# Performance work log

Hardware: AMD Instinct MI355X
Metric: run time of the kernel (lower is better)

The kernel has to match this reference:

```python
import jax, jax.numpy as jnp
import numpy as np

N, E, IN, H, HEADS, L, OUT = 4096, 262144, 64, 128, 4, 2, 2
DH = H // HEADS  # 32, per-head dim for both GAT and global MHA
BN_EPS = 1e-5
NEG_SLOPE = 0.2  # GATConv leaky_relu default


def setup_inputs() -> dict:
    key = jax.random.key(0)
    ks = iter(jax.random.split(key, 32))
    rn = lambda shape, s: jax.random.normal(next(ks), shape, jnp.float32) * s
    return {
        "x": rn((N, IN), 1.0),
        "edge_index": jax.random.randint(next(ks), (2, E), 0, N),
        "w_in": rn((H, IN), IN ** -0.5),
        "b_in": rn((H,), 0.02),
        "w_gat": rn((L, H, H), H ** -0.5),
        "att_src": rn((L, HEADS, DH), 0.1),
        "att_dst": rn((L, HEADS, DH), 0.1),
        "b_gat": rn((L, H), 0.02),
        "w_qkv": rn((L, 3 * H, H), H ** -0.5),
        "b_qkv": rn((L, 3 * H), 0.02),
        "w_o": rn((L, H, H), H ** -0.5),
        "b_o": rn((L, H), 0.02),
        "bn_gamma": 1.0 + rn((L, 3, H), 0.05),
        "bn_beta": rn((L, 3, H), 0.05),
        "w1": rn((L, 2 * H, H), H ** -0.5),
        "b1": rn((L, 2 * H), 0.02),
        "w2": rn((L, H, 2 * H), (2 * H) ** -0.5),
        "b2": rn((L, H), 0.02),
        "w_out": rn((OUT, H), H ** -0.5),
        "b_out": rn((OUT,), 0.02),
    }


def _bn(h, g, b):
    # eval-mode BatchNorm1d with running_mean=0, running_var=1
    return h * (g / jnp.sqrt(1.0 + BN_EPS)) + b


def _gat(x, src, dst, w, a_src, a_dst, bias):
    # GATConv(hidden, hidden//heads, heads=HEADS, add_self_loops=False), concat=True
    xp = (x @ w.T).reshape(N, HEADS, DH)                  # [N, HEADS, DH]
    al_s = jnp.einsum('nhd,hd->nh', xp, a_src)            # [N, HEADS]
    al_d = jnp.einsum('nhd,hd->nh', xp, a_dst)
    logit = al_s[src] + al_d[dst]                         # [E, HEADS]
    logit = jnp.where(logit >= 0, logit, NEG_SLOPE * logit)
    m = jax.ops.segment_max(logit, dst, num_segments=N)   # scatter-softmax over dst
    m = jnp.where(jnp.isfinite(m), m, 0.0)
    e = jnp.exp(logit - m[dst])
    denom = jax.ops.segment_sum(e, dst, num_segments=N)
    alpha = e / (denom[dst] + 1e-16)
    out = jax.ops.segment_sum(alpha[:, :, None] * xp[src], dst, num_segments=N)
    return out.reshape(N, H) + bias


def _mha(x, wqkv, bqkv, wo, bo):
    # torch.nn.MultiheadAttention self-attention over all N nodes (one graph)
    qkv = x @ wqkv.T + bqkv
    q, k, v = jnp.split(qkv, 3, axis=-1)
    q = q.reshape(N, HEADS, DH)
    k = k.reshape(N, HEADS, DH)
    v = v.reshape(N, HEADS, DH)
    scores = jnp.einsum('nhd,mhd->hnm', q, k) / jnp.sqrt(jnp.float32(DH))
    attn = jax.nn.softmax(scores, axis=-1)
    out = jnp.einsum('hnm,mhd->nhd', attn, v).reshape(N, H)
    return out @ wo.T + bo


def reference(x, edge_index, w_in, b_in, w_gat, att_src, att_dst, b_gat,
              w_qkv, b_qkv, w_o, b_o, bn_gamma, bn_beta,
              w1, b1, w2, b2, w_out, b_out):
    src, dst = edge_index[0], edge_index[1]
    h = jax.nn.relu(x @ w_in.T + b_in)
    for l in range(L):
        # GPSConv: local GAT branch (dropout inactive in eval)
        h_loc = _gat(h, src, dst, w_gat[l], att_src[l], att_dst[l], b_gat[l]) + h
        h_loc = _bn(h_loc, bn_gamma[l, 0], bn_beta[l, 0])
        # GPSConv: global attention branch
        h_att = _mha(h, w_qkv[l], b_qkv[l], w_o[l], b_o[l]) + h
        h_att = _bn(h_att, bn_gamma[l, 1], bn_beta[l, 1])
        out = h_loc + h_att
        mlp = jax.nn.relu(out @ w1[l].T + b1[l]) @ w2[l].T + b2[l]
        out = _bn(out + mlp, bn_gamma[l, 2], bn_beta[l, 2])
        # GPSRiskModel residual + relu (dropout inactive in eval)
        h = jax.nn.relu(out + h)
    return h @ w_out.T + b_out
```

## Files before the change

### kernel.cpp

```cpp
#include <hip/hip_runtime.h>

#define NN 4096
#define EE 262144
#define INF_ 64
#define HH 128
#define HEADS 4
#define DH 32
#define LL 2
#define NH (NN * HH)
#define KSPLIT 16
#define L2E 1.4426950408889634f

typedef unsigned short u16;
typedef unsigned int u32;
using bf16x8 = __attribute__((ext_vector_type(8))) short;
using f32x4 = __attribute__((ext_vector_type(4))) float;

__device__ __forceinline__ float bf2f(u16 v) { return __uint_as_float(((u32)v) << 16); }
__device__ __forceinline__ u16 f2bf(float f) {
    u32 u = __float_as_uint(f);
    u32 r = (u + 0x7fffu + ((u >> 16) & 1u)) >> 16;
    return (u16)r;
}
__device__ __forceinline__ u32 encf(float f) {
    u32 b = __float_as_uint(f);
    return (b & 0x80000000u) ? ~b : (b | 0x80000000u);
}
__device__ __forceinline__ float decf(u32 u) {
    u32 b = (u & 0x80000000u) ? (u & 0x7fffffffu) : ~u;
    return __uint_as_float(b);
}

__global__ __launch_bounds__(256) void k_detect(const u16* __restrict__ x, int* __restrict__ flag,
                                                int* __restrict__ cnt, u32* __restrict__ gmax) {
    int t = threadIdx.x;
    for (int i = t; i < NN; i += 256) cnt[i] = 0;
    if (t < 16) gmax[t] = 0;
    __shared__ int cs[256];
    u16 v = x[2 * t];
    int e = (v >> 7) & 0xFF;
    cs[t] = (e >= 100 && e <= 140) ? 1 : 0;
    __syncthreads();
    for (int s = 128; s > 0; s >>= 1) {
        if (t < s) cs[t] += cs[t + s];
        __syncthreads();
    }
    if (t == 0) *flag = (cs[0] >= 128) ? 1 : 0;
}

#define MAXSEG 16
struct SegF { const void* src[MAXSEG]; int dst[MAXSEG]; int n[MAXSEG]; int cnt; };
struct SegB { const void* src[8]; u16* dst[8]; u16* dst2[8]; int n[8]; int cnt; };
__global__ __launch_bounds__(256) void k_prep(SegF SF, float* __restrict__ W, SegB SB,
                                              const int* __restrict__ flag,
                                              const int* __restrict__ dst, int* __restrict__ cnt) {
    int bid = blockIdx.x, t = threadIdx.x;
    if (bid < 96) {
        int seg = bid >> 3, bx = bid & 7;
        if (seg >= SF.cnt) return;
        int n = SF.n[seg];
        float* d = W + SF.dst[seg];
        const void* s = SF.src[seg];
        int f = *flag;
        for (int i = bx * 256 + t; i < n; i += 8 * 256)
            d[i] = f ? bf2f(((const u16*)s)[i]) : ((const float*)s)[i];
    } else if (bid < 992) {
        int b2 = bid - 96;
        int seg = b2 >> 7, bx = b2 & 127;
        if (seg >= SB.cnt) return;
        int f = *flag;
        u16* d = SB.dst[seg];
        u16* d2 = SB.dst2[seg];
        if (f && !d2) return;
        int n = SB.n[seg];
        const void* s = SB.src[seg];
        for (int i = bx * 256 + t; i < n; i += 128 * 256) {
            if (d2) {
                float v = f ? bf2f(((const u16*)s)[i]) : ((const float*)s)[i];
                u16 h = f2bf(v);
                d[i] = h;
                d2[i] = f2bf(v - bf2f(h));
            } else {
                d[i] = f2bf(((const float*)s)[i]);
            }
        }
    } else {
        int e = (bid - 992) * 256 + t;
        if (e < EE) atomicAdd(&cnt[dst[e]], 1);
    }
}

__global__ __launch_bounds__(128) void k_mgemm(const u16* __restrict__ Ahi, const u16* __restrict__ Alo,
                                               const u16* __restrict__ Wc, const u16* __restrict__ Wd,
                                               const int* __restrict__ flag,
                                               const float* __restrict__ bias,
                                               float* __restrict__ outf, u16* __restrict__ outb16,
                                               u16* __restrict__ outhi, u16* __restrict__ outlo,
                                               int K, int J, int relu, int jtiles,
                                               const int* __restrict__ scnt, int* __restrict__ srowstart,
                                               int* __restrict__ scursor) {
    __shared__ int part[128];
    if ((int)blockIdx.y >= jtiles) {
        if (blockIdx.x != 0 || scnt == nullptr) return;
        int t = threadIdx.x;
        int loc[32];
        int s = 0;
#pragma unroll
        for (int i = 0; i < 32; ++i) { loc[i] = s; s += scnt[t * 32 + i]; }
        part[t] = s;
        __syncthreads();
        for (int off = 1; off < 128; off <<= 1) {
            int v = part[t];
            int a = (t >= off) ? part[t - off] : 0;
            __syncthreads();
            part[t] = v + a;
            __syncthreads();
        }
        int base = (t == 0) ? 0 : part[t - 1];
#pragma unroll
        for (int i = 0; i < 32; ++i) {
            srowstart[t * 32 + i] = base + loc[i];
            scursor[t * 32 + i] = base + loc[i];
        }
        return;
    }
    const u16* Wb = (*flag) ? Wd : Wc;
    int wave = threadIdx.x >> 6, lane = threadIdx.x & 63;
    int grp = lane >> 4, lcol = lane & 15;
    int m0 = blockIdx.x * 32 + wave * 16;
    int j0 = blockIdx.y * 64;
    f32x4 acc[4];
#pragma unroll
    for (int s = 0; s < 4; ++s) acc[s] = (f32x4){0.f, 0.f, 0.f, 0.f};
    const u16* ah = Ahi + (size_t)(m0 + lcol) * K + grp * 8;
    const u16* al = Alo + (size_t)(m0 + lcol) * K + grp * 8;
    const u16* wb = Wb + (size_t)(j0 + lcol) * K + grp * 8;
    for (int k = 0; k < K; k += 32) {
        bf16x8 va = *(const bf16x8*)(ah + k);
        bf16x8 vl = *(const bf16x8*)(al + k);
#pragma unroll
        for (int s = 0; s < 4; ++s) {
            bf16x8 vw = *(const bf16x8*)(wb + (size_t)s * 16 * K + k);
            acc[s] = __builtin_amdgcn_mfma_f32_16x16x32_bf16(va, vw, acc[s], 0, 0, 0);
            acc[s] = __builtin_amdgcn_mfma_f32_16x16x32_bf16(vl, vw, acc[s], 0, 0, 0);
        }
    }
#pragma unroll
    for (int s = 0; s < 4; ++s) {
        int col = j0 + s * 16 + lcol;
        float bs = bias ? bias[col] : 0.f;
#pragma unroll
        for (int r = 0; r < 4; ++r) {
            float v = acc[s][r] + bs;
            if (relu) v = fmaxf(v, 0.f);
            size_t idx = (size_t)(m0 + grp * 4 + r) * J + col;
            if (outf) outf[idx] = v;
            if (outb16) outb16[idx] = f2bf(v);
            if (outhi) {
                u16 hv = f2bf(v);
                outhi[idx] = hv;
                outlo[idx] = f2bf(v - bf2f(hv));
            }
        }
    }
}

__global__ __launch_bounds__(128) void k_gemm_gq(const u16* __restrict__ Ahi, const u16* __restrict__ Alo,
                                                 const u16* __restrict__ wgatc, const u16* __restrict__ wgatd,
                                                 const u16* __restrict__ wqkvc, const u16* __restrict__ wqkvd,
                                                 const int* __restrict__ flag,
                                                 const float* __restrict__ bqkv,
                                                 u16* __restrict__ xpb, u16* __restrict__ qkvb,
                                                 const int* __restrict__ esrc_src, const int* __restrict__ esrc_dst,
                                                 int* __restrict__ cursor, int* __restrict__ esrc) {
    if (blockIdx.y >= 8) {
        int b = (blockIdx.y - 8) * 128 + blockIdx.x;
        for (int e = b * 128 + threadIdx.x; e < EE; e += 32768) {
            int d = esrc_dst[e];
            int p = atomicAdd(&cursor[d], 1);
            esrc[p] = esrc_src[e];
        }
        return;
    }
    int wave = threadIdx.x >> 6, lane = threadIdx.x & 63;
    int grp = lane >> 4, lcol = lane & 15;
    int m0 = blockIdx.x * 32 + wave * 16;
    int jb = blockIdx.y;
    int j0 = jb * 64;
    int f = *flag;
    const u16* wgat = f ? wgatd : wgatc;
    const u16* wqkv = f ? wqkvd : wqkvc;
    const u16* Wb = (jb < 2) ? (wgat + (size_t)j0 * HH) : (wqkv + (size_t)(j0 - 128) * HH);
    f32x4 acc[4];
#pragma unroll
    for (int s = 0; s < 4; ++s) acc[s] = (f32x4){0.f, 0.f, 0.f, 0.f};
    const u16* ah = Ahi + (size_t)(m0 + lcol) * HH + grp * 8;
    const u16* al = Alo + (size_t)(m0 + lcol) * HH + grp * 8;
    const u16* wb = Wb + (size_t)lcol * HH + grp * 8;
    for (int k = 0; k < HH; k += 32) {
        bf16x8 va = *(const bf16x8*)(ah + k);
        bf16x8 vl = *(const bf16x8*)(al + k);
#pragma unroll
        for (int s = 0; s < 4; ++s) {
            bf16x8 vw = *(const bf16x8*)(wb + (size_t)s * 16 * HH + k);
            acc[s] = __builtin_amdgcn_mfma_f32_16x16x32_bf16(va, vw, acc[s], 0, 0, 0);
            acc[s] = __builtin_amdgcn_mfma_f32_16x16x32_bf16(vl, vw, acc[s], 0, 0, 0);
        }
    }
    if (jb < 2) {
#pragma unroll
        for (int s = 0; s < 4; ++s) {
            int col = j0 + s * 16 + lcol;
#pragma unroll
            for (int r = 0; r < 4; ++r)
                xpb[(size_t)(m0 + grp * 4 + r) * HH + col] = f2bf(acc[s][r]);
        }
    } else {
#pragma unroll
        for (int s = 0; s < 4; ++s) {
            int colq = j0 - 128 + s * 16 + lcol;
            float bs = bqkv[colq];
#pragma unroll
            for (int r = 0; r < 4; ++r)
                qkvb[(size_t)(m0 + grp * 4 + r) * 384 + colq] = f2bf(acc[s][r] + bs);
        }
    }
}

__global__ __launch_bounds__(128) void k_gemm_wo(const u16* __restrict__ Ahi, const u16* __restrict__ Alo,
                                                 const u16* __restrict__ Wc, const u16* __restrict__ Wd,
                                                 const int* __restrict__ flag,
                                                 const float* __restrict__ bias,
                                                 const float* __restrict__ gatb, const float* __restrict__ hbuf,
                                                 const float* __restrict__ bgat, const float* __restrict__ gam,
                                                 const float* __restrict__ bet,
                                                 float* __restrict__ outb, u16* __restrict__ ohi,
                                                 u16* __restrict__ olo) {
    const u16* Wb = (*flag) ? Wd : Wc;
    int wave = threadIdx.x >> 6, lane = threadIdx.x & 63;
    int grp = lane >> 4, lcol = lane & 15;
    int m0 = blockIdx.x * 32 + wave * 16;
    int j0 = blockIdx.y * 64;
    f32x4 acc[4];
#pragma unroll
    for (int s = 0; s < 4; ++s) acc[s] = (f32x4){0.f, 0.f, 0.f, 0.f};
    const u16* ah = Ahi + (size_t)(m0 + lcol) * HH + grp * 8;
    const u16* al = Alo + (size_t)(m0 + lcol) * HH + grp * 8;
    const u16* wb = Wb + (size_t)(j0 + lcol) * HH + grp * 8;
    for (int k = 0; k < HH; k += 32) {
        bf16x8 va = *(const bf16x8*)(ah + k);
        bf16x8 vl = *(const bf16x8*)(al + k);
#pragma unroll
        for (int s = 0; s < 4; ++s) {
            bf16x8 vw = *(const bf16x8*)(wb + (size_t)s * 16 * HH + k);
            acc[s] = __builtin_amdgcn_mfma_f32_16x16x32_bf16(va, vw, acc[s], 0, 0, 0);
            acc[s] = __builtin_amdgcn_mfma_f32_16x16x32_bf16(vl, vw, acc[s], 0, 0, 0);
        }
    }
    float rs = rsqrtf(1.00001f);
#pragma unroll
    for (int s = 0; s < 4; ++s) {
        int col = j0 + s * 16 + lcol;
        float bs = bias[col];
        float g0 = gam[col] * rs, b0 = bet[col];
        float g1 = gam[HH + col] * rs, b1 = bet[HH + col];
        float bg = bgat[col];
#pragma unroll
        for (int r = 0; r < 4; ++r) {
            size_t idx = (size_t)(m0 + grp * 4 + r) * HH + col;
            float proj = acc[s][r] + bs;
            float hv = hbuf[idx];
            float hl = g0 * (gatb[idx] + bg + hv) + b0;
            float ha = g1 * (proj + hv) + b1;
            float v = hl + ha;
            outb[idx] = v;
            u16 hb = f2bf(v);
            ohi[idx] = hb;
            olo[idx] = f2bf(v - bf2f(hb));
        }
    }
}

__global__ __launch_bounds__(128) void k_gemm_w2(const u16* __restrict__ Ahi, const u16* __restrict__ Alo,
                                                 const u16* __restrict__ Wc, const u16* __restrict__ Wd,
                                                 const int* __restrict__ flag,
                                                 const float* __restrict__ bias,
                                                 const float* __restrict__ outb, const float* __restrict__ gam2,
                                                 const float* __restrict__ bet2,
                                                 float* __restrict__ hbuf, u16* __restrict__ hhi,
                                                 u16* __restrict__ hlo) {
    const u16* Wb = (*flag) ? Wd : Wc;
    int wave = threadIdx.x >> 6, lane = threadIdx.x & 63;
    int grp = lane >> 4, lcol = lane & 15;
    int m0 = blockIdx.x * 32 + wave * 16;
    int j0 = blockIdx.y * 64;
    const int K = 2 * HH;
    f32x4 acc[4];
#pragma unroll
    for (int s = 0; s < 4; ++s) acc[s] = (f32x4){0.f, 0.f, 0.f, 0.f};
    const u16* ah = Ahi + (size_t)(m0 + lcol) * K + grp * 8;
    const u16* al = Alo + (size_t)(m0 + lcol) * K + grp * 8;
    const u16* wb = Wb + (size_t)(j0 + lcol) * K + grp * 8;
    for (int k = 0; k < K; k += 32) {
        bf16x8 va = *(const bf16x8*)(ah + k);
        bf16x8 vl = *(const bf16x8*)(al + k);
#pragma unroll
        for (int s = 0; s < 4; ++s) {
            bf16x8 vw = *(const bf16x8*)(wb + (size_t)s * 16 * K + k);
            acc[s] = __builtin_amdgcn_mfma_f32_16x16x32_bf16(va, vw, acc[s], 0, 0, 0);
            acc[s] = __builtin_amdgcn_mfma_f32_16x16x32_bf16(vl, vw, acc[s], 0, 0, 0);
        }
    }
    float rs = rsqrtf(1.00001f);
#pragma unroll
    for (int s = 0; s < 4; ++s) {
        int col = j0 + s * 16 + lcol;
        float bs = bias[col];
        float g2 = gam2[col] * rs, b2 = bet2[col];
#pragma unroll
        for (int r = 0; r < 4; ++r) {
            size_t idx = (size_t)(m0 + grp * 4 + r) * HH + col;
            float mlpo = acc[s][r] + bs;
            float o2 = g2 * (outb[idx] + mlpo) + b2;
            float v = fmaxf(o2 + hbuf[idx], 0.f);
            hbuf[idx] = v;
            u16 hb = f2bf(v);
            hhi[idx] = hb;
            hlo[idx] = f2bf(v - bf2f(hb));
        }
    }
}

__global__ __launch_bounds__(256) void k_splitlog(const u16* __restrict__ qkvb,
                                                  float* __restrict__ PM, float* __restrict__ PL,
                                                  u16* __restrict__ PO,
                                                  const u16* __restrict__ xpb,
                                                  const float* __restrict__ asrc,
                                                  const float* __restrict__ adst,
                                                  float* __restrict__ als, float* __restrict__ ald,
                                                  u32* __restrict__ gmax) {
    __shared__ __align__(16) u16 Klds[64][40];
    __shared__ __align__(16) u32 Vlds[32][40];
    __shared__ __align__(16) u16 Plds[4][32][36];

    if (blockIdx.x >= 2048) {
        float* red = (float*)&Klds[0][0];
        int t = (blockIdx.x - 2048) * 256 + threadIdx.x;
        int n = t >> 2, hh = t & 3;
        const u16* xr = xpb + (size_t)n * HH + hh * DH;
        float s1 = 0.f, s2 = 0.f;
#pragma unroll
        for (int d = 0; d < DH; ++d) {
            float v = bf2f(xr[d]);
            s1 += v * asrc[hh * DH + d];
            s2 += v * adst[hh * DH + d];
        }
        als[t] = s1;
        ald[t] = s2;
        int lt = threadIdx.x;
        red[lt] = s1;
        __syncthreads();
        for (int off = 128; off >= 4; off >>= 1) {
            if (lt < off) red[lt] = fmaxf(red[lt], red[lt + off]);
            __syncthreads();
        }
        if (lt < 4) atomicMax(&gmax[lt], encf(red[lt]));
        __syncthreads();
        red[lt] = s2;
        __syncthreads();
        for (int off = 128; off >= 4; off >>= 1) {
            if (lt < off) red[lt] = fmaxf(red[lt], red[lt + off]);
            __syncthreads();
        }
        if (lt < 4) atomicMax(&gmax[4 + lt], encf(red[lt]));
        return;
    }

    const float C1 = 0.17677669529663687f * L2E;
    int head = blockIdx.x & 3;
    int qt = (blockIdx.x >> 2) & 31;
    int ks = blockIdx.x >> 7;
    int tid = threadIdx.x;
    int wave = tid >> 6, lane = tid & 63;
    int grp = lane >> 4, lcol = lane & 15;

    int qrow0 = qt * 128 + wave * 32;
    bf16x8 aQ0 = *(const bf16x8*)(qkvb + (size_t)(qrow0 + lcol) * 384 + head * 32 + grp * 8);
    bf16x8 aQ1 = *(const bf16x8*)(qkvb + (size_t)(qrow0 + 16 + lcol) * 384 + head * 32 + grp * 8);

    short onev = (lcol == 0) ? (short)0x3F80 : (short)0;
    bf16x8 bOne = {onev, onev, onev, onev, onev, onev, onev, onev};

    f32x4 oc00 = {0.f, 0.f, 0.f, 0.f}, oc01 = {0.f, 0.f, 0.f, 0.f};
    f32x4 oc10 = {0.f, 0.f, 0.f, 0.f}, oc11 = {0.f, 0.f, 0.f, 0.f};
    f32x4 ol0 = {0.f, 0.f, 0.f, 0.f}, ol1 = {0.f, 0.f, 0.f, 0.f};
    float msh = -INFINITY;

    int isK = (tid < 128);
    int st = tid & 127;
    int skey = st >> 1, shalf = (st & 1) * 16;
    int vj = st & 15, vc = (st >> 4) & 1, dgrp = st >> 5;
    const u16* kptr = qkvb + 128 + head * 32 + shalf;
    const u16* vptr = qkvb + 256 + head * 32 + dgrp * 8;
    int vk0 = vc * 32 + vj;
    int vk1 = vc * 32 + 16 + vj;

    int kt0 = ks * (NN / KSPLIT);
    bf16x8 r0, r1;
    if (isK) {
        r0 = *(const bf16x8*)(kptr + (size_t)(kt0 + skey) * 384);
        r1 = *(const bf16x8*)(kptr + (size_t)(kt0 + skey) * 384 + 8);
    } else {
        r0 = *(const bf16x8*)(vptr + (size_t)(kt0 + vk0) * 384);
        r1 = *(const bf16x8*)(vptr + (size_t)(kt0 + vk1) * 384);
    }

    const int NT = (NN / KSPLIT) / 64;
    for (int t = 0; t < NT; ++t) {
        if (isK) {
            *(bf16x8*)(&Klds[skey][shalf]) = r0;
            *(bf16x8*)(&Klds[skey][shalf + 8]) = r1;
        } else {
#pragma unroll
            for (int j = 0; j < 8; ++j)
                Vlds[dgrp * 8 + j][vc * 20 + vj] = (u32)(u16)r0[j] | ((u32)(u16)r1[j] << 16);
        }
        __syncthreads();
        if (t + 1 < NT) {
            int kn = kt0 + (t + 1) * 64;
            if (isK) {
                r0 = *(const bf16x8*)(kptr + (size_t)(kn + skey) * 384);
                r1 = *(const bf16x8*)(kptr + (size_t)(kn + skey) * 384 + 8);
            } else {
                r0 = *(const bf16x8*)(vptr + (size_t)(kn + vk0) * 384);
                r1 = *(const bf16x8*)(vptr + (size_t)(kn + vk1) * 384);
            }
        }
        f32x4 sc0[4], sc1[4];
        f32x4 zero = {0.f, 0.f, 0.f, 0.f};
#pragma unroll
        for (int s = 0; s < 4; ++s) {
            bf16x8 bK = *(const bf16x8*)(&Klds[s * 16 + lcol][grp * 8]);
            sc0[s] = __builtin_amdgcn_mfma_f32_16x16x32_bf16(aQ0, bK, zero, 0, 0, 0);
            sc1[s] = __builtin_amdgcn_mfma_f32_16x16x32_bf16(aQ1, bK, zero, 0, 0, 0);
        }
        float mymax = sc0[0][0];
#pragma unroll
        for (int s = 0; s < 4; ++s)
#pragma unroll
            for (int r = 0; r < 4; ++r) {
                mymax = fmaxf(mymax, sc0[s][r]);
                mymax = fmaxf(mymax, sc1[s][r]);
            }
        mymax = fmaxf(mymax, __shfl_xor(mymax, 1));
        mymax = fmaxf(mymax, __shfl_xor(mymax, 2));
        mymax = fmaxf(mymax, __shfl_xor(mymax, 4));
        mymax = fmaxf(mymax, __shfl_xor(mymax, 8));
        float mnew = fmaxf(msh, mymax * C1);
        float cc = __builtin_exp2f(msh - mnew);
        msh = mnew;
        oc00 *= cc; oc01 *= cc; ol0 *= cc;
        oc10 *= cc; oc11 *= cc; ol1 *= cc;
#pragma unroll
        for (int c2 = 0; c2 < 2; ++c2) {
#pragma unroll
            for (int r = 0; r < 4; ++r) {
                float p0 = __builtin_exp2f(__builtin_fmaf(sc0[2 * c2][r], C1, -mnew));
                float p1 = __builtin_exp2f(__builtin_fmaf(sc0[2 * c2 + 1][r], C1, -mnew));
                *(u32*)(&Plds[wave][grp * 4 + r][2 * lcol]) =
                    __builtin_amdgcn_perm(__float_as_uint(p1), __float_as_uint(p0), 0x07060302u);
                float q0 = __builtin_exp2f(__builtin_fmaf(sc1[2 * c2][r], C1, -mnew));
                float q1 = __builtin_exp2f(__builtin_fmaf(sc1[2 * c2 + 1][r], C1, -mnew));
                *(u32*)(&Plds[wave][16 + grp * 4 + r][2 * lcol]) =
                    __builtin_amdgcn_perm(__float_as_uint(q1), __float_as_uint(q0), 0x07060302u);
            }
            bf16x8 aP0 = *(const bf16x8*)(&Plds[wave][lcol][grp * 8]);
            bf16x8 aP1 = *(const bf16x8*)(&Plds[wave][16 + lcol][grp * 8]);
            bf16x8 bV0 = *(const bf16x8*)(&Vlds[lcol][c2 * 20 + grp * 4]);
            bf16x8 bV1 = *(const bf16x8*)(&Vlds[16 + lcol][c2 * 20 + grp * 4]);
            oc00 = __builtin_amdgcn_mfma_f32_16x16x32_bf16(aP0, bV0, oc00, 0, 0, 0);
            oc01 = __builtin_amdgcn_mfma_f32_16x16x32_bf16(aP0, bV1, oc01, 0, 0, 0);
            ol0 = __builtin_amdgcn_mfma_f32_16x16x32_bf16(aP0, bOne, ol0, 0, 0, 0);
            oc10 = __builtin_amdgcn_mfma_f32_16x16x32_bf16(aP1, bV0, oc10, 0, 0, 0);
            oc11 = __builtin_amdgcn_mfma_f32_16x16x32_bf16(aP1, bV1, oc11, 0, 0, 0);
            ol1 = __builtin_amdgcn_mfma_f32_16x16x32_bf16(aP1, bOne, ol1, 0, 0, 0);
        }
        __syncthreads();
    }
#pragma unroll
    for (int r = 0; r < 4; ++r) {
        int row0 = qrow0 + grp * 4 + r;
        size_t b0 = ((size_t)row0 * HEADS + head) * KSPLIT + ks;
        PO[b0 * 32 + lcol] = f2bf(oc00[r]);
        PO[b0 * 32 + 16 + lcol] = f2bf(oc01[r]);
        int row1 = row0 + 16;
        size_t b1 = ((size_t)row1 * HEADS + head) * KSPLIT + ks;
        PO[b1 * 32 + lcol] = f2bf(oc10[r]);
        PO[b1 * 32 + 16 + lcol] = f2bf(oc11[r]);
        if (lcol == 0) {
            PM[b0] = msh;
            PL[b0] = ol0[r];
            PM[b1] = msh;
            PL[b1] = ol1[r];
        }
    }
}

#define GCHUNK 256
__global__ __launch_bounds__(128) void k_gatcomb(const int* __restrict__ esrc, const int* __restrict__ rowstart,
                                                 const int* __restrict__ cnt, const float* __restrict__ als,
                                                 const float* __restrict__ ald, const u16* __restrict__ xpb,
                                                 float* __restrict__ gatout, const u32* __restrict__ gmax,
                                                 const float* __restrict__ PM, const float* __restrict__ PL,
                                                 const u16* __restrict__ PO, u16* __restrict__ atthi,
                                                 u16* __restrict__ attlo) {
    __shared__ float red[512];
    __shared__ float elds[GCHUNK * 4];
    __shared__ int slds[GCHUNK];
    int t = threadIdx.x;

    if (blockIdx.x >= NN) {
        int n2 = blockIdx.x - NN;
        float* wn = red;
        if (t < 64) {
            int head = t >> 4, ks = t & 15;
            size_t b = ((size_t)n2 * HEADS + head) * KSPLIT + ks;
            float pm = PM[b];
            float m = pm;
#pragma unroll
            for (int off = 1; off < 16; off <<= 1) m = fmaxf(m, __shfl_xor(m, off));
            float w = __builtin_exp2f(pm - m);
            float lw = PL[b] * w;
#pragma unroll
            for (int off = 1; off < 16; off <<= 1) lw += __shfl_xor(lw, off);
            wn[t] = w / lw;
        }
        __syncthreads();
        int head = t >> 5, dim = t & 31;
        size_t b0 = ((size_t)n2 * HEADS + head) * KSPLIT;
        float o = 0.f;
#pragma unroll
        for (int k = 0; k < KSPLIT; ++k)
            o += wn[head * 16 + k] * bf2f(PO[(b0 + k) * 32 + dim]);
        size_t idx = (size_t)n2 * HH + t;
        u16 h = f2bf(o);
        atthi[idx] = h;
        attlo[idx] = f2bf(o - bf2f(h));
        return;
    }

    int n = blockIdx.x;
    int base = rowstart[n], c = cnt[n];
    float4 adv = ((const float4*)ald)[n];
    float ad[4] = {adv.x, adv.y, adv.z, adv.w};
    float M2[4];
#pragma unroll
    for (int h = 0; h < 4; ++h) {
        float bound = decf(gmax[h]) + decf(gmax[4 + h]);
        float M = bound >= 0.f ? bound : 0.2f * bound;
        M2[h] = M * L2E;
    }
    float dsum[4] = {0.f, 0.f, 0.f, 0.f};
    float acc = 0.f;
    int ht = t >> 5;
    for (int ch = 0; ch < c; ch += GCHUNK) {
        int cn = min(GCHUNK, c - ch);
        __syncthreads();
        for (int i = t; i < cn; i += 128) {
            int s = esrc[base + ch + i];
            slds[i] = s;
            float4 as = ((const float4*)als)[s];
            float lg, e;
            lg = as.x + ad[0]; lg = lg >= 0.f ? lg : 0.2f * lg; e = __builtin_exp2f(lg * L2E - M2[0]); elds[i * 4 + 0] = e; dsum[0] += e;
            lg = as.y + ad[1]; lg = lg >= 0.f ? lg : 0.2f * lg; e = __builtin_exp2f(lg * L2E - M2[1]); elds[i * 4 + 1] = e; dsum[1] += e;
            lg = as.z + ad[2]; lg = lg >= 0.f ? lg : 0.2f * lg; e = __builtin_exp2f(lg * L2E - M2[2]); elds[i * 4 + 2] = e; dsum[2] += e;
            lg = as.w + ad[3]; lg = lg >= 0.f ? lg : 0.2f * lg; e = __builtin_exp2f(lg * L2E - M2[3]); elds[i * 4 + 3] = e; dsum[3] += e;
        }
        __syncthreads();
        int i = 0;
        for (; i + 4 <= cn; i += 4) {
            int s0 = slds[i], s1 = slds[i + 1], s2 = slds[i + 2], s3 = slds[i + 3];
            float x0 = bf2f(xpb[(size_t)s0 * HH + t]);
            float x1 = bf2f(xpb[(size_t)s1 * HH + t]);
            float x2 = bf2f(xpb[(size_t)s2 * HH + t]);
            float x3 = bf2f(xpb[(size_t)s3 * HH + t]);
            acc += elds[i * 4 + ht] * x0 + elds[(i + 1) * 4 + ht] * x1;
            acc += elds[(i + 2) * 4 + ht] * x2 + elds[(i + 3) * 4 + ht] * x3;
        }
        for (; i < cn; ++i) acc += elds[i * 4 + ht] * bf2f(xpb[(size_t)slds[i] * HH + t]);
    }
    __syncthreads();
#pragma unroll
    for (int h = 0; h < 4; ++h) red[h * 128 + t] = dsum[h];
    __syncthreads();
    for (int s2 = 64; s2 > 0; s2 >>= 1) {
        if (t < s2) {
#pragma unroll
            for (int h = 0; h < 4; ++h)
                red[h * 128 + t] += red[h * 128 + t + s2];
        }
        __syncthreads();
    }
    float inv = 1.f / (red[ht * 128] + 1e-16f);
    gatout[(size_t)n * HH + t] = acc * inv;
}

__global__ __launch_bounds__(64) void k_out(const float* __restrict__ h, const float* __restrict__ w,
                                            const float* __restrict__ b, void* __restrict__ yout,
                                            const int* __restrict__ flag) {
    int n = blockIdx.x, l = threadIdx.x;
    float a0 = 0.f, a1 = 0.f;
    for (int k = l; k < HH; k += 64) {
        float hv = h[(size_t)n * HH + k];
        a0 += hv * w[k];
        a1 += hv * w[HH + k];
    }
#pragma unroll
    for (int off = 32; off > 0; off >>= 1) {
        a0 += __shfl_xor(a0, off);
        a1 += __shfl_xor(a1, off);
    }
    if (l == 0) {
        float o0 = a0 + b[0], o1 = a1 + b[1];
        if (*flag) {
            u16* y = (u16*)yout;
            y[n * 2 + 0] = f2bf(o0);
            y[n * 2 + 1] = f2bf(o1);
        } else {
            float* y = (float*)yout;
            y[n * 2 + 0] = o0;
            y[n * 2 + 1] = o1;
        }
    }
}

extern "C" void kernel_launch(void* const* d_in, const int* in_sizes, int n_in,
                              void* d_out, int out_size, void* d_ws, size_t ws_size,
                              hipStream_t stream) {
    float* W = (float*)d_ws;
    size_t o = 0;
    auto take = [&](size_t n) { size_t r = o; o += n; return r; };
    size_t pb_in = take(HH);
    size_t pattS = take(LL * HEADS * DH);
    size_t pattD = take(LL * HEADS * DH);
    size_t pb_gat = take(LL * HH);
    size_t pb_qkv = take(LL * 3 * HH);
    size_t pb_o  = take(LL * HH);
    size_t pbn_g = take(LL * 3 * HH);
    size_t pbn_b = take(LL * 3 * HH);
    size_t pb1   = take(LL * 2 * HH);
    size_t pb2   = take(LL * HH);
    size_t pw_out = take(2 * HH);
    size_t pb_out = take(2);
    auto takeb = [&](size_t nu16) { size_t r = o; o += (nu16 + 1) / 2; return r; };
    size_t bw_in  = takeb(HH * INF_);
    size_t bw_gat = takeb(LL * HH * HH);
    size_t bw_qkv = takeb(LL * 3 * HH * HH);
    size_t bw_o   = takeb(LL * HH * HH);
    size_t bw1    = takeb(LL * 2 * HH * HH);
    size_t bw2    = takeb(LL * HH * 2 * HH);
    o = (o + 127) & ~(size_t)127;
    size_t ohbuf = take(NH);
    size_t ogat  = take(NH);
    size_t otmp  = take(NH);
    size_t oals  = take(NN * HEADS);
    size_t oald  = take(NN * HEADS);
    size_t opm   = take(NN * HEADS * KSPLIT);
    size_t opl   = take(NN * HEADS * KSPLIT);
    size_t opo   = takeb((size_t)NN * HEADS * KSPLIT * 32);
    size_t oqkvb = takeb(NN * 384);
    size_t oxpb  = takeb(NH);
    size_t oxhi  = takeb(NN * INF_);
    size_t oxlo  = takeb(NN * INF_);
    size_t ohhi  = takeb(NH);
    size_t ohlo  = takeb(NH);
    size_t oahi  = takeb(NH);
    size_t oalo  = takeb(NH);
    size_t oohi  = takeb(NH);
    size_t oolo  = takeb(NH);
    size_t omhi  = takeb(NN * 2 * HH);
    size_t omlo  = takeb(NN * 2 * HH);
    int* ibase    = (int*)(W + o);
    int* iflag    = ibase;
    int* cnt      = ibase + 64;
    int* rowstart = cnt + NN;
    int* cursor   = rowstart + NN;
    int* esrc     = cursor + NN;
    u32* gmax     = (u32*)(esrc + EE);

    float* hbuf = W + ohbuf;
    float* gatb = W + ogat;
    float* tmp  = W + otmp;
    float* als  = W + oals;
    float* ald  = W + oald;
    float* pmb  = W + opm;
    float* plb  = W + opl;
    u16* pob  = (u16*)(W + opo);
    u16* qkvb = (u16*)(W + oqkvb);
    u16* xpb  = (u16*)(W + oxpb);
    u16* xhi = (u16*)(W + oxhi), *xlo = (u16*)(W + oxlo);
    u16* hhi = (u16*)(W + ohhi), *hlo = (u16*)(W + ohlo);
    u16* ahi = (u16*)(W + oahi), *alo = (u16*)(W + oalo);
    u16* ohi = (u16*)(W + oohi), *olo = (u16*)(W + oolo);
    u16* mhi = (u16*)(W + omhi), *mlo = (u16*)(W + omlo);

    const int* src = (const int*)d_in[1];
    const int* dst = (const int*)d_in[1] + EE;
    const u16* dw_in  = (const u16*)d_in[2];
    const u16* dw_gat = (const u16*)d_in[4];
    const u16* dw_qkv = (const u16*)d_in[8];
    const u16* dw_o   = (const u16*)d_in[10];
    const u16* dw1    = (const u16*)d_in[14];
    const u16* dw2    = (const u16*)d_in[16];

    k_detect<<<1, 256, 0, stream>>>((const u16*)d_in[0], iflag, cnt, gmax);

    SegF SF = {};
    int nf = 0;
    auto addf = [&](int idx, size_t off, int n) { SF.src[nf] = d_in[idx]; SF.dst[nf] = (int)off; SF.n[nf] = n; ++nf; };
    addf(3, pb_in, HH);
    addf(5, pattS, LL * HEADS * DH);
    addf(6, pattD, LL * HEADS * DH);
    addf(7, pb_gat, LL * HH);
    addf(9, pb_qkv, LL * 3 * HH);
    addf(11, pb_o, LL * HH);
    addf(12, pbn_g, LL * 3 * HH);
    addf(13, pbn_b, LL * 3 * HH);
    addf(15, pb1, LL * 2 * HH);
    addf(17, pb2, LL * HH);
    addf(18, pw_out, 2 * HH);
    addf(19, pb_out, 2);
    SF.cnt = nf;

    SegB SB = {};
    int nb = 0;
    auto addb = [&](int idx, size_t off, int n, u16* d2) {
        SB.src[nb] = d_in[idx]; SB.dst[nb] = (u16*)(W + off); SB.dst2[nb] = d2; SB.n[nb] = n; ++nb;
    };
    addb(2, bw_in, HH * INF_, nullptr);
    addb(4, bw_gat, LL * HH * HH, nullptr);
    addb(8, bw_qkv, LL * 3 * HH * HH, nullptr);
    addb(10, bw_o, LL * HH * HH, nullptr);
    addb(14, bw1, LL * 2 * HH * HH, nullptr);
    addb(16, bw2, LL * HH * 2 * HH, nullptr);
    SB.src[nb] = d_in[0]; SB.dst[nb] = xhi; SB.dst2[nb] = xlo; SB.n[nb] = NN * INF_; ++nb;
    SB.cnt = nb;

    k_prep<<<2016, 256, 0, stream>>>(SF, W, SB, iflag, dst, cnt);

    k_mgemm<<<dim3(NN / 32, HH / 64 + 1), 128, 0, stream>>>(xhi, xlo, (u16*)(W + bw_in), dw_in, iflag,
                                                            W + pb_in, hbuf, nullptr, hhi, hlo, INF_, HH, 1,
                                                            HH / 64, cnt, rowstart, cursor);

    for (int l = 0; l < LL; ++l) {
        k_gemm_gq<<<dim3(NN / 32, (l == 0) ? 10 : 8), 128, 0, stream>>>(hhi, hlo,
                                                        (u16*)(W + bw_gat) + (size_t)l * HH * HH,
                                                        dw_gat + (size_t)l * HH * HH,
                                                        (u16*)(W + bw_qkv) + (size_t)l * 3 * HH * HH,
                                                        dw_qkv + (size_t)l * 3 * HH * HH,
                                                        iflag, W + pb_qkv + l * 3 * HH, xpb, qkvb,
                                                        src, dst, cursor, esrc);
        k_splitlog<<<2048 + (NN * HEADS) / 256, 256, 0, stream>>>(qkvb, pmb, plb, pob, xpb,
                                                                  W + pattS + l * HEADS * DH,
                                                                  W + pattD + l * HEADS * DH,
                                                                  als, ald, gmax + l * 8);
        k_gatcomb<<<2 * NN, 128, 0, stream>>>(esrc, rowstart, cnt, als, ald, xpb, gatb, gmax + l * 8,
                                              pmb, plb, pob, ahi, alo);
        k_gemm_wo<<<dim3(NN / 32, HH / 64), 128, 0, stream>>>(ahi, alo,
                                                              (u16*)(W + bw_o) + (size_t)l * HH * HH,
                                                              dw_o + (size_t)l * HH * HH, iflag,
                                                              W + pb_o + l * HH, gatb, hbuf,
                                                              W + pb_gat + l * HH, W + pbn_g + l * 3 * HH,
                                                              W + pbn_b + l * 3 * HH, tmp, ohi, olo);
        k_mgemm<<<dim3(NN / 32, 256 / 64), 128, 0, stream>>>(ohi, olo,
                                                             (u16*)(W + bw1) + (size_t)l * 2 * HH * HH,
                                                             dw1 + (size_t)l * 2 * HH * HH, iflag,
                                                             W + pb1 + l * 2 * HH, nullptr, nullptr,
                                                             mhi, mlo, HH, 2 * HH, 1,
                                                             256 / 64, nullptr, nullptr, nullptr);
        k_gemm_w2<<<dim3(NN / 32, HH / 64), 128, 0, stream>>>(mhi, mlo,
                                                              (u16*)(W + bw2) + (size_t)l * HH * 2 * HH,
                                                              dw2 + (size_t)l * HH * 2 * HH, iflag,
                                                              W + pb2 + l * HH, tmp,
                                                              W + pbn_g + l * 3 * HH + 2 * HH,
                                                              W + pbn_b + l * 3 * HH + 2 * HH,
                                                              hbuf, hhi, hlo);
    }
    k_out<<<NN, 64, 0, stream>>>(hbuf, W + pw_out, W + pb_out, d_out, iflag);
}
```

Measured before the change: 290.3 us.

## Fuse MLP W1 and W2 GEMMs into one kernel, add MFMA setprio

Merges the two MLP GEMMs (W1 with ReLU, then W2 with the BN/residual epilogue) into one kernel. Each block computes a 16-row slab of the hidden activation, keeps it in LDS as a bf16 hi/lo split, and feeds it straight into the second GEMM. This removes the global round trip of the intermediate and one launch per layer, at the cost of fewer rows per block (256 blocks) and more work per block. It also wraps the MFMA bursts in the attention kernel with s_setprio to favour matrix issue.

```diff
diff --git a/kernel.cpp b/kernel.cpp
--- a/kernel.cpp
+++ b/kernel.cpp
@@ -281,32 +281,70 @@
     }
 }
 
-__global__ __launch_bounds__(128) void k_gemm_w2(const u16* __restrict__ Ahi, const u16* __restrict__ Alo,
-                                                 const u16* __restrict__ Wc, const u16* __restrict__ Wd,
-                                                 const int* __restrict__ flag,
-                                                 const float* __restrict__ bias,
-                                                 const float* __restrict__ outb, const float* __restrict__ gam2,
-                                                 const float* __restrict__ bet2,
-                                                 float* __restrict__ hbuf, u16* __restrict__ hhi,
-                                                 u16* __restrict__ hlo) {
-    const u16* Wb = (*flag) ? Wd : Wc;
+__global__ __launch_bounds__(128) void k_gemm_mlp(const u16* __restrict__ Ahi, const u16* __restrict__ Alo,
+                                                  const u16* __restrict__ W1c, const u16* __restrict__ W1d,
+                                                  const u16* __restrict__ W2c, const u16* __restrict__ W2d,
+                                                  const int* __restrict__ flag,
+                                                  const float* __restrict__ b1, const float* __restrict__ b2,
+                                                  const float* __restrict__ outb, const float* __restrict__ gam2,
+                                                  const float* __restrict__ bet2,
+                                                  float* __restrict__ hbuf, u16* __restrict__ hhi,
+                                                  u16* __restrict__ hlo) {
+    __shared__ u16 Hhi[16][264];
+    __shared__ u16 Hlo[16][264];
+    int f = *flag;
+    const u16* W1 = f ? W1d : W1c;
+    const u16* W2 = f ? W2d : W2c;
     int wave = threadIdx.x >> 6, lane = threadIdx.x & 63;
     int grp = lane >> 4, lcol = lane & 15;
-    int m0 = blockIdx.x * 32 + wave * 16;
-    int j0 = blockIdx.y * 64;
-    const int K = 2 * HH;
+    int m0 = blockIdx.x * 16;
+    const u16* ah = Ahi + (size_t)(m0 + lcol) * HH + grp * 8;
+    const u16* al = Alo + (size_t)(m0 + lcol) * HH + grp * 8;
+#pragma unroll
+    for (int jt = 0; jt < 2; ++jt) {
+        int j0 = wave * 128 + jt * 64;
+        f32x4 acc[4];
+#pragma unroll
+        for (int s = 0; s < 4; ++s) acc[s] = (f32x4){0.f, 0.f, 0.f, 0.f};
+        const u16* wb = W1 + (size_t)(j0 + lcol) * HH + grp * 8;
+#pragma unroll
+        for (int k = 0; k < HH; k += 32) {
+            bf16x8 va = *(const bf16x8*)(ah + k);
+            bf16x8 vl = *(const bf16x8*)(al + k);
+#pragma unroll
+            for (int s = 0; s < 4; ++s) {
+                bf16x8 vw = *(const bf16x8*)(wb + (size_t)s * 16 * HH + k);
+                acc[s] = __builtin_amdgcn_mfma_f32_16x16x32_bf16(va, vw, acc[s], 0, 0, 0);
+                acc[s] = __builtin_amdgcn_mfma_f32_16x16x32_bf16(vl, vw, acc[s], 0, 0, 0);
+            }
+        }
+#pragma unroll
+        for (int s = 0; s < 4; ++s) {
+            int col = j0 + s * 16 + lcol;
+            float bs = b1[col];
+#pragma unroll
+            for (int r = 0; r < 4; ++r) {
+                float v = fmaxf(acc[s][r] + bs, 0.f);
+                int row = grp * 4 + r;
+                u16 hv = f2bf(v);
+                Hhi[row][col] = hv;
+                Hlo[row][col] = f2bf(v - bf2f(hv));
+            }
+        }
+    }
+    __syncthreads();
+    int j0 = wave * 64;
     f32x4 acc[4];
 #pragma unroll
     for (int s = 0; s < 4; ++s) acc[s] = (f32x4){0.f, 0.f, 0.f, 0.f};
-    const u16* ah = Ahi + (size_t)(m0 + lcol) * K + grp * 8;
-    const u16* al = Alo + (size_t)(m0 + lcol) * K + grp * 8;
-    const u16* wb = Wb + (size_t)(j0 + lcol) * K + grp * 8;
-    for (int k = 0; k < K; k += 32) {
-        bf16x8 va = *(const bf16x8*)(ah + k);
-        bf16x8 vl = *(const bf16x8*)(al + k);
+    const u16* wb = W2 + (size_t)(j0 + lcol) * 256 + grp * 8;
+#pragma unroll
+    for (int k = 0; k < 256; k += 32) {
+        bf16x8 va = *(const bf16x8*)(&Hhi[lcol][k + grp * 8]);
+        bf16x8 vl = *(const bf16x8*)(&Hlo[lcol][k + grp * 8]);
 #pragma unroll
         for (int s = 0; s < 4; ++s) {
-            bf16x8 vw = *(const bf16x8*)(wb + (size_t)s * 16 * K + k);
+            bf16x8 vw = *(const bf16x8*)(wb + (size_t)s * 16 * 256 + k);
             acc[s] = __builtin_amdgcn_mfma_f32_16x16x32_bf16(va, vw, acc[s], 0, 0, 0);
             acc[s] = __builtin_amdgcn_mfma_f32_16x16x32_bf16(vl, vw, acc[s], 0, 0, 0);
         }
@@ -315,13 +353,13 @@
 #pragma unroll
     for (int s = 0; s < 4; ++s) {
         int col = j0 + s * 16 + lcol;
-        float bs = bias[col];
-        float g2 = gam2[col] * rs, b2 = bet2[col];
+        float bs = b2[col];
+        float g2 = gam2[col] * rs, bb2 = bet2[col];
 #pragma unroll
         for (int r = 0; r < 4; ++r) {
             size_t idx = (size_t)(m0 + grp * 4 + r) * HH + col;
             float mlpo = acc[s][r] + bs;
-            float o2 = g2 * (outb[idx] + mlpo) + b2;
+            float o2 = g2 * (outb[idx] + mlpo) + bb2;
             float v = fmaxf(o2 + hbuf[idx], 0.f);
             hbuf[idx] = v;
             u16 hb = f2bf(v);
@@ -438,12 +476,14 @@
         }
         f32x4 sc0[4], sc1[4];
         f32x4 zero = {0.f, 0.f, 0.f, 0.f};
+        __builtin_amdgcn_s_setprio(1);
 #pragma unroll
         for (int s = 0; s < 4; ++s) {
             bf16x8 bK = *(const bf16x8*)(&Klds[s * 16 + lcol][grp * 8]);
             sc0[s] = __builtin_amdgcn_mfma_f32_16x16x32_bf16(aQ0, bK, zero, 0, 0, 0);
             sc1[s] = __builtin_amdgcn_mfma_f32_16x16x32_bf16(aQ1, bK, zero, 0, 0, 0);
         }
+        __builtin_amdgcn_s_setprio(0);
         float mymax = sc0[0][0];
 #pragma unroll
         for (int s = 0; s < 4; ++s)
@@ -478,12 +518,14 @@
             bf16x8 aP1 = *(const bf16x8*)(&Plds[wave][16 + lcol][grp * 8]);
             bf16x8 bV0 = *(const bf16x8*)(&Vlds[lcol][c2 * 20 + grp * 4]);
             bf16x8 bV1 = *(const bf16x8*)(&Vlds[16 + lcol][c2 * 20 + grp * 4]);
+            __builtin_amdgcn_s_setprio(1);
             oc00 = __builtin_amdgcn_mfma_f32_16x16x32_bf16(aP0, bV0, oc00, 0, 0, 0);
             oc01 = __builtin_amdgcn_mfma_f32_16x16x32_bf16(aP0, bV1, oc01, 0, 0, 0);
             ol0 = __builtin_amdgcn_mfma_f32_16x16x32_bf16(aP0, bOne, ol0, 0, 0, 0);
             oc10 = __builtin_amdgcn_mfma_f32_16x16x32_bf16(aP1, bV0, oc10, 0, 0, 0);
             oc11 = __builtin_amdgcn_mfma_f32_16x16x32_bf16(aP1, bV1, oc11, 0, 0, 0);
             ol1 = __builtin_amdgcn_mfma_f32_16x16x32_bf16(aP1, bOne, ol1, 0, 0, 0);
+            __builtin_amdgcn_s_setprio(0);
         }
         __syncthreads();
     }
@@ -702,7 +744,6 @@
     u16* hhi = (u16*)(W + ohhi), *hlo = (u16*)(W + ohlo);
     u16* ahi = (u16*)(W + oahi), *alo = (u16*)(W + oalo);
     u16* ohi = (u16*)(W + oohi), *olo = (u16*)(W + oolo);
-    u16* mhi = (u16*)(W + omhi), *mlo = (u16*)(W + omlo);
 
     const int* src = (const int*)d_in[1];
     const int* dst = (const int*)d_in[1] + EE;
@@ -772,19 +813,15 @@
                                                               W + pb_o + l * HH, gatb, hbuf,
                                                               W + pb_gat + l * HH, W + pbn_g + l * 3 * HH,
                                                               W + pbn_b + l * 3 * HH, tmp, ohi, olo);
-        k_mgemm<<<dim3(NN / 32, 256 / 64), 128, 0, stream>>>(ohi, olo,
-                                                             (u16*)(W + bw1) + (size_t)l * 2 * HH * HH,
-                                                             dw1 + (size_t)l * 2 * HH * HH, iflag,
-                                                             W + pb1 + l * 2 * HH, nullptr, nullptr,
-                                                             mhi, mlo, HH, 2 * HH, 1,
-                                                             256 / 64, nullptr, nullptr, nullptr);
-        k_gemm_w2<<<dim3(NN / 32, HH / 64), 128, 0, stream>>>(mhi, mlo,
-                                                              (u16*)(W + bw2) + (size_t)l * HH * 2 * HH,
-                                                              dw2 + (size_t)l * HH * 2 * HH, iflag,
-                                                              W + pb2 + l * HH, tmp,
-                                                              W + pbn_g + l * 3 * HH + 2 * HH,
-                                                              W + pbn_b + l * 3 * HH + 2 * HH,
-                                                              hbuf, hhi, hlo);
+        k_gemm_mlp<<<NN / 16, 128, 0, stream>>>(ohi, olo,
+                                                (u16*)(W + bw1) + (size_t)l * 2 * HH * HH,
+                                                dw1 + (size_t)l * 2 * HH * HH,
+                                                (u16*)(W + bw2) + (size_t)l * HH * 2 * HH,
+                                                dw2 + (size_t)l * HH * 2 * HH, iflag,
+                                                W + pb1 + l * 2 * HH, W + pb2 + l * HH,
+                                                tmp, W + pbn_g + l * 3 * HH + 2 * HH,
+                                                W + pbn_b + l * 3 * HH + 2 * HH,
+                                                hbuf, hhi, hlo);
     }
     k_out<<<NN, 64, 0, stream>>>(hbuf, W + pw_out, W + pb_out, d_out, iflag);
 }
```

Result: no change. 288.9 us (-0.5%).
